# Kernel tuning notes

Measured on AMD Instinct MI355X. Metric: run time of the kernel, lower is better.

The kernel has to match this reference:

```python
import jax, jax.numpy as jnp
import numpy as np

B = 16
T_LEN, T_DIM = 149, 768
H = W = 56
S_DIM = 512
EPS = 1e-5


def setup_inputs() -> dict:
    key = jax.random.key(0)
    ks = jax.random.split(key, 12)
    N = H * W  # 3136
    return {
        "x": jax.random.normal(ks[0], (B, T_LEN, T_DIM), dtype=jnp.float32),
        "y": jax.random.normal(ks[1], (B, S_DIM, H, W), dtype=jnp.float32),
        # Conv1d(time_len -> h*w, k=1)
        "W_conv1": jax.random.normal(ks[2], (N, T_LEN), dtype=jnp.float32) * (1.0 / np.sqrt(T_LEN)),
        "b_conv1": jnp.zeros((N,), dtype=jnp.float32),
        # LayerNorms
        "ln1_g": jnp.ones((T_DIM,), dtype=jnp.float32),
        "ln1_b": jnp.zeros((T_DIM,), dtype=jnp.float32),
        "ln2_g": jnp.ones((S_DIM,), dtype=jnp.float32),
        "ln2_b": jnp.zeros((S_DIM,), dtype=jnp.float32),
        # positional encodings (1, C, H, W)
        "pe_wave": jax.random.normal(ks[3], (1, T_DIM, H, W), dtype=jnp.float32) * 0.02,
        "pe_spec": jax.random.normal(ks[4], (1, S_DIM, H, W), dtype=jnp.float32) * 0.02,
        # CrossAttention2D 1x1 convs
        "Wq": jax.random.normal(ks[5], (S_DIM, T_DIM), dtype=jnp.float32) * (1.0 / np.sqrt(T_DIM)),
        "bq": jnp.zeros((S_DIM,), dtype=jnp.float32),
        "Wk": jax.random.normal(ks[6], (S_DIM, S_DIM), dtype=jnp.float32) * (1.0 / np.sqrt(S_DIM)),
        "bk": jnp.zeros((S_DIM,), dtype=jnp.float32),
    }


def _layernorm(t, g, b):
    # t: (..., C), normalized over last axis
    m = jnp.mean(t, axis=-1, keepdims=True)
    v = jnp.mean(jnp.square(t - m), axis=-1, keepdims=True)
    return (t - m) * jax.lax.rsqrt(v + EPS) * g + b


def reference(x, y, W_conv1, b_conv1, ln1_g, ln1_b, ln2_g, ln2_b,
              pe_wave, pe_spec, Wq, bq, Wk, bk):
    # conv1d k=1 over channel dim time_len: (B,149,768) -> (B,3136,768)
    xe = jnp.einsum('bld,ol->bod', x, W_conv1) + b_conv1[None, :, None]
    # rearrange 'b (h w) c -> b h w c' (channel-last for LN/attention)
    nx = xe.reshape(x.shape[0], H, W, T_DIM)
    nx = _layernorm(nx, ln1_g, ln1_b) + pe_wave.transpose(0, 2, 3, 1)  # (B,H,W,768)

    ny = y.transpose(0, 2, 3, 1)  # (B,H,W,512)
    ny = _layernorm(ny, ln2_g, ln2_b) + pe_spec.transpose(0, 2, 3, 1)

    # 1x1 convs -> q, k; value is norm_y itself
    q = jnp.einsum('bhwc,oc->bhwo', nx, Wq) + bq  # (B,H,W,512)
    k = jnp.einsum('bhwc,oc->bhwo', ny, Wk) + bk  # (B,H,W,512)
    v = ny

    # row-local attention: each (b,h) row of W=56 tokens attends within itself
    scores = jnp.einsum('bhqc,bhkc->bhqk', q, k) / jnp.sqrt(jnp.float32(S_DIM))
    attn = jax.nn.softmax(scores, axis=-1)  # (B,H,W,W)
    out = jnp.einsum('bhqk,bhkc->bhqc', attn, v)  # (B,H,W,512)

    # permute back to (B,C,H,W), residual add
    return out.transpose(0, 3, 1, 2) + y
```

## Files before the change

kernel.cpp:

```cpp
#include <hip/hip_runtime.h>
#include <hip/hip_bf16.h>
#include <math.h>

typedef short bf16x8 __attribute__((ext_vector_type(8)));
typedef float f32x4 __attribute__((ext_vector_type(4)));

#define LN_EPS 1e-5f

static __device__ __forceinline__ float b2f(unsigned short u){
  unsigned int x = ((unsigned int)u) << 16; float f; __builtin_memcpy(&f,&x,4); return f;
}
static __device__ __forceinline__ unsigned short f2b(float f){
  unsigned int x; __builtin_memcpy(&x,&f,4);
  x += 0x7fffu + ((x>>16)&1u);
  return (unsigned short)(x>>16);
}

static __device__ __forceinline__ void gload_lds16(const void* g, void* l){
  __builtin_amdgcn_global_load_lds(
      (const __attribute__((address_space(1))) unsigned int*)g,
      (__attribute__((address_space(3))) unsigned int*)l, 16, 0, 0);
}

__global__ void pack_rowpad(const float* __restrict__ src, unsigned short* __restrict__ dst,
                            int rows, int srcK, int dstK, int rowsPad){
  int idx = blockIdx.x*256 + threadIdx.x;
  if (idx >= rowsPad*dstK) return;
  int r = idx / dstK, kk = idx - r*dstK;
  float v = (r < rows && kk < srcK) ? src[(size_t)r*srcK + kk] : 0.f;
  dst[idx] = f2b(v);
}

__global__ __launch_bounds__(256) void pack_xt(const float* __restrict__ x, unsigned short* __restrict__ xt){
  __shared__ float tile[32][33];
  int b = blockIdx.z;
  int l0 = blockIdx.y*32, d0 = blockIdx.x*32;
  int tl = threadIdx.x & 31, tw = threadIdx.x >> 5;
  for (int r=0;r<32;r+=8){
    int l = l0 + tw + r;
    tile[tw+r][tl] = (l<149) ? x[((size_t)b*149 + l)*768 + d0 + tl] : 0.f;
  }
  __syncthreads();
  for (int r=0;r<32;r+=8){
    int d = d0 + tw + r;
    int l = l0 + tl;
    if (l < 160) xt[((size_t)b*768 + d)*160 + l] = f2b(tile[tl][tw+r]);
  }
}

__global__ __launch_bounds__(256) void transpose_pe(const float* __restrict__ src, float* __restrict__ dst, int C){
  __shared__ float tile[32][33];
  int c0 = blockIdx.y*32, o0 = blockIdx.x*32;
  int tl = threadIdx.x & 31, tw = threadIdx.x >> 5;
  for (int r=0;r<32;r+=8)
    tile[tw+r][tl] = src[(size_t)(c0+tw+r)*3136 + o0 + tl];
  __syncthreads();
  for (int r=0;r<32;r+=8)
    dst[(size_t)(o0+tw+r)*C + c0 + tl] = tile[tl][tw+r];
}

#define GBM 128
#define GBN 128
#define GBK 32
__global__ __launch_bounds__(256)
void gemm_nt(const unsigned short* __restrict__ A, const unsigned short* __restrict__ Bt,
             unsigned short* __restrict__ C, const float* __restrict__ bias,
             int M, int N, int K, long long aStride, long long bStride, long long cStride,
             int swz8){
  __shared__ __align__(16) unsigned short As[GBM*GBK];
  __shared__ __align__(16) unsigned short Bs[GBN*GBK];
  int bx = blockIdx.x, by = blockIdx.y;
  if (swz8){
    int id = bx + gridDim.x*by;
    int xcd = id & 7, s = id >> 3;
    int q = s / gridDim.y;
    bx = xcd*(gridDim.x >> 3) + q;
    by = s - q*gridDim.y;
  }
  const unsigned short* Ab = A + (size_t)blockIdx.z*aStride;
  const unsigned short* Bb = Bt + (size_t)blockIdx.z*bStride;
  unsigned short* Cb = C + (size_t)blockIdx.z*cStride;
  int m0 = bx*GBM, n0 = by*GBN;
  int tid = threadIdx.x;
  int lane = tid & 63, wave = tid >> 6;
  int wm = (wave >> 1)*64, wn = (wave & 1)*64;
  f32x4 acc[4][4];
  #pragma unroll
  for (int i=0;i<4;i++)
    #pragma unroll
    for (int j=0;j<4;j++) acc[i][j]=(f32x4){0.f,0.f,0.f,0.f};
  int lr = lane & 15, lk = (lane >> 4)*8;
  for (int k0 = 0; k0 < K; k0 += GBK){
    #pragma unroll
    for (int p2=0;p2<2;p2++){
      int i = p2*256 + wave*64 + lane;
      gload_lds16(Ab + (size_t)(m0 + (i>>2))*K + k0 + (i&3)*8, As + (size_t)(p2*256 + wave*64)*8);
    }
    #pragma unroll
    for (int p2=0;p2<2;p2++){
      int i = p2*256 + wave*64 + lane;
      gload_lds16(Bb + (size_t)(n0 + (i>>2))*K + k0 + (i&3)*8, Bs + (size_t)(p2*256 + wave*64)*8);
    }
    __syncthreads();
    bf16x8 af[4], bfr[4];
    #pragma unroll
    for (int mi=0;mi<4;mi++) af[mi]  = *reinterpret_cast<const bf16x8*>(&As[(wm + mi*16 + lr)*GBK + lk]);
    #pragma unroll
    for (int nj=0;nj<4;nj++) bfr[nj] = *reinterpret_cast<const bf16x8*>(&Bs[(wn + nj*16 + lr)*GBK + lk]);
    #pragma unroll
    for (int mi=0;mi<4;mi++)
      #pragma unroll
      for (int nj=0;nj<4;nj++)
        acc[mi][nj] = __builtin_amdgcn_mfma_f32_16x16x32_bf16(af[mi], bfr[nj], acc[mi][nj], 0, 0, 0);
    __syncthreads();
  }
  int er = (lane >> 4)*4;
  #pragma unroll
  for (int mi=0;mi<4;mi++)
    #pragma unroll
    for (int nj=0;nj<4;nj++){
      int col = n0 + wn + nj*16 + lr;
      float bv = bias ? bias[col] : 0.f;
      #pragma unroll
      for (int e=0;e<4;e++){
        int row = m0 + wm + mi*16 + er + e;
        if (row < M) Cb[(size_t)row*N + col] = f2b(acc[mi][nj][e] + bv);
      }
    }
}

#define MFMA16(a,b,c) __builtin_amdgcn_mfma_f32_16x16x32_bf16(a,b,c,0,0,0)
__global__ __launch_bounds__(512)
void gemm256(const unsigned short* __restrict__ A, const unsigned short* __restrict__ Bt,
             unsigned short* __restrict__ C, const float* __restrict__ bias,
             int M, int N, int K){
  __shared__ __align__(16) unsigned short lds[65536];
  int tid = threadIdx.x;
  int lane = tid & 63, wave = tid >> 6;
  int wr = wave >> 2, wc = wave & 3;
  int lr = lane & 15, lo = lane >> 4;
  int cpx = gridDim.x >> 3;
  int id = blockIdx.x;
  int sid = (id & 7)*cpx + (id >> 3);
  int nby = N >> 8;
  int bx = sid / nby, by = sid - bx*nby;
  int m0 = bx << 8, n0 = by << 8;
  int NT = K >> 6;

  f32x4 acc[8][4];
  #pragma unroll
  for (int i=0;i<8;i++)
    #pragma unroll
    for (int j=0;j<4;j++) acc[i][j]=(f32x4){0.f,0.f,0.f,0.f};

  auto STAGE = [&](int t, int h){
    if (t >= NT) return;
    int buf = t & 1, tensor = h >> 1, half = h & 1;
    int k0 = t << 6;
    unsigned short* dstbase = lds + buf*32768 + tensor*16384;
    const unsigned short* srcT = tensor ? (Bt + (size_t)n0*K) : (A + (size_t)m0*K);
    #pragma unroll
    for (int ldi=0; ldi<2; ldi++){
      int c = half*1024 + ldi*512 + tid;
      int r = c >> 3;
      int l = (c & 7) ^ (r & 7);
      gload_lds16(srcT + (size_t)r*K + k0 + l*8,
                  dstbase + (half*1024 + ldi*512 + (wave<<6))*8);
    }
  };
  const char* ldsc = reinterpret_cast<const char*>(lds);
  int swz = lr & 7;
  auto rdA = [&](int buf, int mi, int kk)->bf16x8{
    int off = buf*65536 + (wr*128 + mi*16 + lr)*128 + (((kk*4+lo) ^ swz)*16);
    return *reinterpret_cast<const bf16x8*>(ldsc + off);
  };
  auto rdB = [&](int buf, int nj, int kk)->bf16x8{
    int off = buf*65536 + 32768 + (wc*64 + nj*16 + lr)*128 + (((kk*4+lo) ^ swz)*16);
    return *reinterpret_cast<const bf16x8*>(ldsc + off);
  };

  STAGE(0,0); STAGE(0,1); STAGE(0,2); STAGE(0,3);
  asm volatile("s_waitcnt vmcnt(0)" ::: "memory");
  __builtin_amdgcn_s_barrier();

  for (int t=0; t<NT; ++t){
    int buf = t & 1;
    STAGE(t+1,0); STAGE(t+1,1); STAGE(t+1,2); STAGE(t+1,3);
    bf16x8 bfr[4][2], af[4][2];
    #pragma unroll
    for (int nj=0;nj<4;nj++){ bfr[nj][0]=rdB(buf,nj,0); bfr[nj][1]=rdB(buf,nj,1); }
    #pragma unroll
    for (int i=0;i<4;i++){ af[i][0]=rdA(buf,i,0); af[i][1]=rdA(buf,i,1); }
    asm volatile("s_waitcnt lgkmcnt(0)" ::: "memory");
    __builtin_amdgcn_s_setprio(1);
    #pragma unroll
    for (int i=0;i<4;i++)
      #pragma unroll
      for (int nj=0;nj<4;nj++){
        acc[i][nj] = MFMA16(af[i][0], bfr[nj][0], acc[i][nj]);
        acc[i][nj] = MFMA16(af[i][1], bfr[nj][1], acc[i][nj]);
      }
    __builtin_amdgcn_s_setprio(0);
    #pragma unroll
    for (int i=0;i<4;i++){ af[i][0]=rdA(buf,4+i,0); af[i][1]=rdA(buf,4+i,1); }
    asm volatile("s_waitcnt lgkmcnt(0)" ::: "memory");
    __builtin_amdgcn_s_setprio(1);
    #pragma unroll
    for (int i=0;i<4;i++)
      #pragma unroll
      for (int nj=0;nj<4;nj++){
        acc[4+i][nj] = MFMA16(af[i][0], bfr[nj][0], acc[4+i][nj]);
        acc[4+i][nj] = MFMA16(af[i][1], bfr[nj][1], acc[4+i][nj]);
      }
    __builtin_amdgcn_s_setprio(0);
    asm volatile("s_waitcnt vmcnt(0)" ::: "memory");
    __builtin_amdgcn_s_barrier();
  }

  int er = lo*4;
  #pragma unroll
  for (int nj=0;nj<4;nj++){
    int col = n0 + wc*64 + nj*16 + lr;
    float bv = bias ? bias[col] : 0.f;
    #pragma unroll
    for (int mi=0;mi<8;mi++){
      int row = m0 + wr*128 + mi*16 + er;
      #pragma unroll
      for (int e=0;e<4;e++)
        C[(size_t)(row+e)*N + col] = f2b(acc[mi][nj][e] + bv);
    }
  }
}

__global__ __launch_bounds__(256) void ln1_kernel(unsigned short* __restrict__ xe,
    const float* __restrict__ g, const float* __restrict__ be, const float* __restrict__ pet){
  int b = blockIdx.y;
  int o0 = blockIdx.x*8;
  int t = threadIdx.x;
  int lane = t & 63, wv = t >> 6;
  __shared__ float ws1[4], ws2[4];
  __shared__ float mArr[8], rArr[8];
  float vals[8][3];
  #pragma unroll
  for (int oi=0;oi<8;oi++){
    size_t base = ((size_t)b*3136 + o0 + oi)*768;
    #pragma unroll
    for (int j=0;j<3;j++) vals[oi][j] = b2f(xe[base + t + 256*j]);
  }
  #pragma unroll
  for (int oi=0;oi<8;oi++){
    float s1=0.f, s2=0.f;
    #pragma unroll
    for (int j=0;j<3;j++){ float v=vals[oi][j]; s1+=v; s2+=v*v; }
    for (int d=32; d>0; d>>=1){ s1 += __shfl_xor(s1,d); s2 += __shfl_xor(s2,d); }
    if (lane==0){ ws1[wv]=s1; ws2[wv]=s2; }
    __syncthreads();
    if (t==0){
      float a=ws1[0]+ws1[1]+ws1[2]+ws1[3];
      float c=ws2[0]+ws2[1]+ws2[2]+ws2[3];
      float m=a*(1.f/768.f);
      float var=c*(1.f/768.f)-m*m;
      mArr[oi]=m; rArr[oi]=rsqrtf(var+LN_EPS);
    }
    __syncthreads();
  }
  #pragma unroll
  for (int oi=0;oi<8;oi++){
    size_t base = ((size_t)b*3136 + o0 + oi)*768;
    size_t pb = (size_t)(o0+oi)*768;
    float m=mArr[oi], r=rArr[oi];
    #pragma unroll
    for (int j=0;j<3;j++){
      int d = t + 256*j;
      xe[base+d] = f2b((vals[oi][j]-m)*r*g[d] + be[d] + pet[pb+d]);
    }
  }
}

__global__ __launch_bounds__(256) void ln2_kernel(const float* __restrict__ y,
    unsigned short* __restrict__ ny, unsigned short* __restrict__ nyT,
    const float* __restrict__ g, const float* __restrict__ bb, const float* __restrict__ pe){
  int b = blockIdx.y;
  int o0 = blockIdx.x*32;
  int t = threadIdx.x;
  int oi = t & 31, cg = t >> 5;
  __shared__ float red1[8][33], red2[8][33];
  __shared__ float mArr[32], rArr[32];
  __shared__ unsigned short tile[32][520];
  size_t ybase = (size_t)b*512*3136 + o0;
  float vals[64];
  float s1=0.f, s2=0.f;
  #pragma unroll
  for (int ci=0; ci<64; ci++){
    int c = cg*64 + ci;
    float v = y[ybase + (size_t)c*3136 + oi];
    vals[ci] = v;
    s1 += v; s2 += v*v;
  }
  red1[cg][oi]=s1; red2[cg][oi]=s2;
  __syncthreads();
  if (t < 32){
    float a=0.f, c2=0.f;
    #pragma unroll
    for (int kk=0;kk<8;kk++){ a+=red1[kk][t]; c2+=red2[kk][t]; }
    float m=a*(1.f/512.f);
    float var=c2*(1.f/512.f)-m*m;
    mArr[t]=m; rArr[t]=rsqrtf(var+LN_EPS);
  }
  __syncthreads();
  float m = mArr[oi], r = rArr[oi];
  #pragma unroll
  for (int ci=0; ci<64; ci++){
    int c = cg*64 + ci;
    float v = (vals[ci]-m)*r*g[c] + bb[c] + pe[(size_t)c*3136 + o0 + oi];
    tile[oi][c] = f2b(v);
  }
  __syncthreads();
  size_t nybase = ((size_t)b*3136 + o0)*512;
  for (int p = t; p < 32*64; p += 256){
    int oo = p >> 6, cp = (p & 63)*8;
    *reinterpret_cast<uint4*>(ny + nybase + (size_t)oo*512 + cp) =
        *reinterpret_cast<const uint4*>(&tile[oo][cp]);
  }
  for (int c2 = t; c2 < 512; c2 += 256){
    unsigned short row[32];
    #pragma unroll
    for (int o=0;o<32;o++) row[o] = tile[o][c2];
    size_t a = ((size_t)b*512 + c2)*3136 + o0;
    #pragma unroll
    for (int u=0;u<4;u++)
      *reinterpret_cast<uint4*>(nyT + a + u*8) = *reinterpret_cast<const uint4*>(&row[u*8]);
  }
}

__global__ __launch_bounds__(256) void attn_kernel(const unsigned short* __restrict__ q,
    const unsigned short* __restrict__ k, const unsigned short* __restrict__ vT,
    unsigned short* __restrict__ outp){
  int h = blockIdx.x, b = blockIdx.y;
  int tid = threadIdx.x;
  int lane = tid & 63, w = tid >> 6;
  size_t base = (size_t)b*3136 + (size_t)h*56;
  __shared__ __align__(16) float Sf[56][60];
  __shared__ __align__(16) unsigned short Sb[64*64];

  f32x4 acc[4];
  #pragma unroll
  for (int mi=0;mi<4;mi++) acc[mi]=(f32x4){0.f,0.f,0.f,0.f};
  int lr = lane & 15, lo = lane >> 4;
  int lk = lo*8;
  int kr = w*16 + lr; if (kr > 55) kr = 55;
  const unsigned short* krow = k + (base + kr)*512;
  for (int k0=0;k0<512;k0+=32){
    bf16x8 kf = *reinterpret_cast<const bf16x8*>(krow + k0 + lk);
    #pragma unroll
    for (int mi=0;mi<4;mi++){
      int qr = mi*16 + lr; if (qr > 55) qr = 55;
      bf16x8 qf = *reinterpret_cast<const bf16x8*>(q + (base+qr)*512 + k0 + lk);
      acc[mi] = __builtin_amdgcn_mfma_f32_16x16x32_bf16(qf, kf, acc[mi], 0,0,0);
    }
  }
  const float scale = 0.04419417382415922f;
  int col = w*16 + lr;
  int er = lo*4;
  if (col < 56){
    #pragma unroll
    for (int mi=0;mi<4;mi++)
      #pragma unroll
      for (int e=0;e<4;e++){
        int row = mi*16 + er + e;
        if (row < 56) Sf[row][col] = acc[mi][e]*scale;
      }
  }
  __syncthreads();

  for (int r=0;r<14;r++){
    int i = w*14 + r;
    float xv = (lane<56) ? Sf[i][lane] : -1e30f;
    float mx = xv;
    #pragma unroll
    for (int d=32; d>0; d>>=1) mx = fmaxf(mx, __shfl_xor(mx,d));
    float ev = (lane<56) ? __expf(xv-mx) : 0.f;
    float sm = ev;
    #pragma unroll
    for (int d=32; d>0; d>>=1) sm += __shfl_xor(sm,d);
    unsigned short pv = (lane<56) ? f2b(ev/sm) : (unsigned short)0;
    int bo = i*128 + ((lane*2) ^ ((i&7)<<4));
    *reinterpret_cast<unsigned short*>(reinterpret_cast<char*>(Sb) + bo) = pv;
  }
  __syncthreads();

  const unsigned short* vb = vT + (size_t)b*512*3136 + (size_t)h*56;
  #pragma unroll
  for (int pass=0; pass<2; ++pass){
    int nbase = w*128 + pass*64;
    bf16x8 bfr[2][4], af[2][4];
    #pragma unroll
    for (int kt=0;kt<2;++kt)
      #pragma unroll
      for (int nj=0;nj<4;++nj){
        int d = nbase + nj*16 + lr;
        bfr[kt][nj] = *reinterpret_cast<const bf16x8*>(vb + (size_t)d*3136 + kt*32 + lk);
      }
    #pragma unroll
    for (int kt=0;kt<2;++kt)
      #pragma unroll
      for (int mi=0;mi<4;++mi){
        int row = mi*16 + lr;
        int bo = row*128 + (((kt*64) + lo*16) ^ ((row&7)<<4));
        af[kt][mi] = *reinterpret_cast<const bf16x8*>(reinterpret_cast<const char*>(Sb) + bo);
      }
    f32x4 a2[4][4];
    #pragma unroll
    for (int mi=0;mi<4;mi++)
      #pragma unroll
      for (int nj=0;nj<4;nj++) a2[mi][nj]=(f32x4){0.f,0.f,0.f,0.f};
    #pragma unroll
    for (int kt=0;kt<2;++kt)
      #pragma unroll
      for (int mi=0;mi<4;++mi)
        #pragma unroll
        for (int nj=0;nj<4;++nj)
          a2[mi][nj] = __builtin_amdgcn_mfma_f32_16x16x32_bf16(af[kt][mi], bfr[kt][nj], a2[mi][nj], 0,0,0);
    #pragma unroll
    for (int mi=0;mi<4;++mi)
      #pragma unroll
      for (int nj=0;nj<4;++nj)
        #pragma unroll
        for (int e=0;e<4;++e){
          int row = mi*16 + er + e;
          if (row < 56)
            outp[(base+row)*512 + nbase + nj*16 + lr] = f2b(a2[mi][nj][e]);
        }
  }
}

__global__ __launch_bounds__(256) void out_kernel(const unsigned short* __restrict__ att,
    const float* __restrict__ y, float* __restrict__ outp){
  __shared__ float tile[32][33];
  int b = blockIdx.z, c0 = blockIdx.y*32, o0 = blockIdx.x*32;
  int tl = threadIdx.x & 31, tw = threadIdx.x >> 5;
  for (int r=0;r<32;r+=8)
    tile[tw+r][tl] = b2f(att[((size_t)b*3136 + o0 + tw + r)*512 + c0 + tl]);
  __syncthreads();
  for (int r=0;r<32;r+=8){
    size_t idx = ((size_t)b*512 + c0 + tw + r)*3136 + o0 + tl;
    outp[idx] = tile[tl][tw+r] + y[idx];
  }
}

extern "C" void kernel_launch(void* const* d_in, const int* in_sizes, int n_in,
                              void* d_out, int out_size, void* d_ws, size_t ws_size,
                              hipStream_t stream){
  const float* x   = (const float*)d_in[0];
  const float* y   = (const float*)d_in[1];
  const float* Wc  = (const float*)d_in[2];
  const float* g1  = (const float*)d_in[4];
  const float* be1 = (const float*)d_in[5];
  const float* g2  = (const float*)d_in[6];
  const float* be2 = (const float*)d_in[7];
  const float* peW = (const float*)d_in[8];
  const float* peS = (const float*)d_in[9];
  const float* Wq  = (const float*)d_in[10];
  const float* bq  = (const float*)d_in[11];
  const float* Wk  = (const float*)d_in[12];
  const float* bk  = (const float*)d_in[13];
  float* outp = (float*)d_out;

  char* p = (char*)d_ws;
  auto alloc = [&](size_t bytes)->char*{ char* r = p; p += (bytes + 255) & ~(size_t)255; return r; };
  unsigned short* WcB = (unsigned short*)alloc((size_t)3200*160*2);
  unsigned short* xt  = (unsigned short*)alloc((size_t)16*768*160*2);
  unsigned short* WqB = (unsigned short*)alloc((size_t)512*768*2);
  unsigned short* WkB = (unsigned short*)alloc((size_t)512*512*2);
  float* peWt = (float*)alloc((size_t)3136*768*4);
  unsigned short* xe  = (unsigned short*)alloc((size_t)16*3136*768*2);
  unsigned short* ny  = (unsigned short*)alloc((size_t)16*3136*512*2);
  unsigned short* nyT = (unsigned short*)alloc((size_t)16*512*3136*2 + 256);
  unsigned short* qb  = (unsigned short*)alloc((size_t)16*3136*512*2);
  unsigned short* kb  = (unsigned short*)alloc((size_t)16*3136*512*2);

  pack_rowpad<<<dim3((3200*160+255)/256), 256, 0, stream>>>(Wc, WcB, 3136, 149, 160, 3200);
  pack_rowpad<<<dim3((512*768+255)/256), 256, 0, stream>>>(Wq, WqB, 512, 768, 768, 512);
  pack_rowpad<<<dim3((512*512+255)/256), 256, 0, stream>>>(Wk, WkB, 512, 512, 512, 512);
  pack_xt<<<dim3(24,5,16), 256, 0, stream>>>(x, xt);
  transpose_pe<<<dim3(98,24), 256, 0, stream>>>(peW, peWt, 768);

  gemm_nt<<<dim3(25,6,16), 256, 0, stream>>>(WcB, xt, xe, nullptr, 3136, 768, 160,
                                             0LL, 768LL*160LL, 3136LL*768LL, 0);
  ln1_kernel<<<dim3(392,16), 256, 0, stream>>>(xe, g1, be1, peWt);
  ln2_kernel<<<dim3(98,16), 256, 0, stream>>>(y, ny, nyT, g2, be2, peS);
  gemm256<<<dim3(392), 512, 0, stream>>>(xe, WqB, qb, bq, 50176, 512, 768);
  gemm256<<<dim3(392), 512, 0, stream>>>(ny, WkB, kb, bk, 50176, 512, 512);
  attn_kernel<<<dim3(56,16), 256, 0, stream>>>(qb, kb, nyT, qb);
  out_kernel<<<dim3(98,16,16), 256, 0, stream>>>(qb, y, outp);
}
```

Baseline: 423.3 us.

## Fuse residual add and NCHW transpose into attention kernel epilogue

The attention kernel now writes its output directly in (B,C,H,W) fp32 layout, adding y in the epilogue through a per-wave LDS transpose tile. This removes the separate out_kernel and the bf16 round trip of the attention output through global memory. V fragments are also loaded earlier, before the softmax, so their global latency overlaps the score and softmax work. The costs are higher register pressure from holding all V fragments, extra LDS, and strided 56-element global writes per channel row.

```diff
diff --git a/kernel.cpp b/kernel.cpp
--- a/kernel.cpp
+++ b/kernel.cpp
@@ -335,13 +335,14 @@
 
 __global__ __launch_bounds__(256) void attn_kernel(const unsigned short* __restrict__ q,
     const unsigned short* __restrict__ k, const unsigned short* __restrict__ vT,
-    unsigned short* __restrict__ outp){
+    const float* __restrict__ y, float* __restrict__ outp){
   int h = blockIdx.x, b = blockIdx.y;
   int tid = threadIdx.x;
   int lane = tid & 63, w = tid >> 6;
   size_t base = (size_t)b*3136 + (size_t)h*56;
   __shared__ __align__(16) float Sf[56][60];
   __shared__ __align__(16) unsigned short Sb[64*64];
+  __shared__ __align__(16) float T[4][16*68];
 
   f32x4 acc[4];
   #pragma unroll
@@ -359,6 +360,19 @@
       acc[mi] = __builtin_amdgcn_mfma_f32_16x16x32_bf16(qf, kf, acc[mi], 0,0,0);
     }
   }
+
+  const unsigned short* vb = vT + (size_t)b*512*3136 + (size_t)h*56;
+  bf16x8 vfr[2][2][4];
+  #pragma unroll
+  for (int pass=0; pass<2; ++pass)
+    #pragma unroll
+    for (int kt=0;kt<2;++kt)
+      #pragma unroll
+      for (int nj=0;nj<4;++nj){
+        int d = w*128 + pass*64 + nj*16 + lr;
+        vfr[pass][kt][nj] = *reinterpret_cast<const bf16x8*>(vb + (size_t)d*3136 + kt*32 + lk);
+      }
+
   const float scale = 0.04419417382415922f;
   int col = w*16 + lr;
   int er = lo*4;
@@ -389,18 +403,11 @@
   }
   __syncthreads();
 
-  const unsigned short* vb = vT + (size_t)b*512*3136 + (size_t)h*56;
+  float* Tw = &T[w][0];
   #pragma unroll
   for (int pass=0; pass<2; ++pass){
     int nbase = w*128 + pass*64;
-    bf16x8 bfr[2][4], af[2][4];
-    #pragma unroll
-    for (int kt=0;kt<2;++kt)
-      #pragma unroll
-      for (int nj=0;nj<4;++nj){
-        int d = nbase + nj*16 + lr;
-        bfr[kt][nj] = *reinterpret_cast<const bf16x8*>(vb + (size_t)d*3136 + kt*32 + lk);
-      }
+    bf16x8 af[2][4];
     #pragma unroll
     for (int kt=0;kt<2;++kt)
       #pragma unroll
@@ -420,31 +427,23 @@
       for (int mi=0;mi<4;++mi)
         #pragma unroll
         for (int nj=0;nj<4;++nj)
-          a2[mi][nj] = __builtin_amdgcn_mfma_f32_16x16x32_bf16(af[kt][mi], bfr[kt][nj], a2[mi][nj], 0,0,0);
-    #pragma unroll
-    for (int mi=0;mi<4;++mi)
-      #pragma unroll
-      for (int nj=0;nj<4;++nj)
+          a2[mi][nj] = __builtin_amdgcn_mfma_f32_16x16x32_bf16(af[kt][mi], vfr[pass][kt][nj], a2[mi][nj], 0,0,0);
+    #pragma unroll
+    for (int nj=0;nj<4;++nj){
+      asm volatile("s_waitcnt lgkmcnt(0)" ::: "memory");
+      __builtin_amdgcn_sched_barrier(0);
+      #pragma unroll
+      for (int mi=0;mi<4;++mi)
+        *reinterpret_cast<f32x4*>(&Tw[lr*68 + mi*16 + er]) = a2[mi][nj];
+      asm volatile("s_waitcnt lgkmcnt(0)" ::: "memory");
+      __builtin_amdgcn_sched_barrier(0);
+      if (lane < 56){
+        size_t gb = ((size_t)b*512 + nbase + nj*16)*3136 + (size_t)h*56 + lane;
         #pragma unroll
-        for (int e=0;e<4;++e){
-          int row = mi*16 + er + e;
-          if (row < 56)
-            outp[(base+row)*512 + nbase + nj*16 + lr] = f2b(a2[mi][nj][e]);
-        }
-  }
-}
-
-__global__ __launch_bounds__(256) void out_kernel(const unsigned short* __restrict__ att,
-    const float* __restrict__ y, float* __restrict__ outp){
-  __shared__ float tile[32][33];
-  int b = blockIdx.z, c0 = blockIdx.y*32, o0 = blockIdx.x*32;
-  int tl = threadIdx.x & 31, tw = threadIdx.x >> 5;
-  for (int r=0;r<32;r+=8)
-    tile[tw+r][tl] = b2f(att[((size_t)b*3136 + o0 + tw + r)*512 + c0 + tl]);
-  __syncthreads();
-  for (int r=0;r<32;r+=8){
-    size_t idx = ((size_t)b*512 + c0 + tw + r)*3136 + o0 + tl;
-    outp[idx] = tile[tl][tw+r] + y[idx];
+        for (int dd=0; dd<16; ++dd)
+          outp[gb + (size_t)dd*3136] = Tw[dd*68 + lane] + y[gb + (size_t)dd*3136];
+      }
+    }
   }
 }
 
@@ -491,6 +490,5 @@
   ln2_kernel<<<dim3(98,16), 256, 0, stream>>>(y, ny, nyT, g2, be2, peS);
   gemm256<<<dim3(392), 512, 0, stream>>>(xe, WqB, qb, bq, 50176, 512, 768);
   gemm256<<<dim3(392), 512, 0, stream>>>(ny, WkB, kb, bk, 50176, 512, 512);
-  attn_kernel<<<dim3(56,16), 256, 0, stream>>>(qb, kb, nyT, qb);
-  out_kernel<<<dim3(98,16,16), 256, 0, stream>>>(qb, y, outp);
-}
+  attn_kernel<<<dim3(56,16), 256, 0, stream>>>(qb, kb, nyT, y, outp);
+}
```

After: 419.3 us. About the same (-0.9%).
